# Optimization experiments

Measured on AMD Instinct MI355X. Metric: run time of the kernel, lower is better.

The kernel has to match this reference:

```python
import jax, jax.numpy as jnp
import numpy as np

B, H, W, DIM = 2, 128, 128, 256
NB, EXP, HEADS = 16, 8, 8
BS = DIM // NB          # AFNO block size = 16
DH = DIM // HEADS       # head dim = 32
EPS = 1e-5
LAM = 0.01              # softshrink threshold


def _ln(x, g, b):
    mu = jnp.mean(x, axis=-1, keepdims=True)
    var = jnp.mean((x - mu) ** 2, axis=-1, keepdims=True)
    return (x - mu) * jax.lax.rsqrt(var + EPS) * g + b


def _afno(x, w1, b1, w2, b2):
    # FourCastNet AFNO2D: block-diagonal complex MLP in Fourier space
    bias = x
    Bx, Hx, Wx, C = x.shape
    xf = jnp.fft.rfft2(x, axes=(1, 2), norm='ortho')          # [B,H,W//2+1,C] complex
    xf = xf.reshape(Bx, Hx, Wx // 2 + 1, NB, BS)
    xr, xi = jnp.real(xf), jnp.imag(xf)
    mm = lambda t, w: jnp.einsum('bhwni,nio->bhwno', t, w)
    o1r = jax.nn.relu(mm(xr, w1[0]) - mm(xi, w1[1]) + b1[0])
    o1i = jax.nn.relu(mm(xi, w1[0]) + mm(xr, w1[1]) + b1[1])
    o2r = mm(o1r, w2[0]) - mm(o1i, w2[1]) + b2[0]
    o2i = mm(o1i, w2[0]) + mm(o1r, w2[1]) + b2[1]
    shrink = lambda t: jnp.sign(t) * jnp.maximum(jnp.abs(t) - LAM, 0.0)
    xf = (shrink(o2r) + 1j * shrink(o2i)).reshape(Bx, Hx, Wx // 2 + 1, C)
    out = jnp.fft.irfft2(xf, s=(Hx, Wx), axes=(1, 2), norm='ortho')
    return out + bias


def _galerkin(h, wq, bq, wk, bk, wv, bv, lnk_g, lnk_b, lnv_g, lnv_b, wo, bo):
    # softmax-free linear attention: Q (LN(K)^T LN(V)) / N
    Bx, N, C = h.shape
    split = lambda t, w, b: (t @ w.T + b).reshape(Bx, N, HEADS, DH).transpose(0, 2, 1, 3)
    q = split(h, wq, bq)
    k = split(h, wk, bk)
    v = split(h, wv, bv)
    k = _ln(k, lnk_g[None, :, None, :], lnk_b[None, :, None, :])
    v = _ln(v, lnv_g[None, :, None, :], lnv_b[None, :, None, :])
    kv = jnp.einsum('bhnd,bhne->bhde', k, v) / N     # [B,h,dh,dh]
    out = jnp.einsum('bhnd,bhde->bhne', q, kv)       # [B,h,N,dh]
    out = out.transpose(0, 2, 1, 3).reshape(Bx, N, C)
    return out @ wo.T + bo


def _forward(x, afno_w1, afno_b1, afno_w2, afno_b2,
             wq, bq, wk, bk, wv, bv, lnk_g, lnk_b, lnv_g, lnv_b, wo, bo,
             w_up, b_up, w_down, b_down,
             n1_g, n1_b, n2_g, n2_b, n3_g, n3_b):
    Bx, Hx, Wx, C = x.shape
    # 1) AFNO spectral mixing block
    x = x + _afno(_ln(x, n1_g, n1_b), afno_w1, afno_b1, afno_w2, afno_b2)
    # 2) Galerkin linear attention block
    x = _ln(x, n2_g, n2_b)
    h = x.reshape(Bx, Hx * Wx, C)
    x = x + _galerkin(h, wq, bq, wk, bk, wv, bv,
                      lnk_g, lnk_b, lnv_g, lnv_b, wo, bo).reshape(Bx, Hx, Wx, C)
    # 3) pointwise-conv (1x1) FFN block; conv1x1 over BCHW == per-token linear in BHWC
    x = _ln(x, n3_g, n3_b)
    h = jax.nn.gelu(x @ w_up.T + b_up, approximate=False)
    x = x + h @ w_down.T + b_down
    return x


def setup_inputs() -> dict:
    key = jax.random.key(0)
    ks = jax.random.split(key, 24)
    r = lambda i, shape, s: jax.random.normal(ks[i], shape, dtype=jnp.float32) * s
    z = lambda shape: jnp.zeros(shape, dtype=jnp.float32)
    o = lambda shape: jnp.ones(shape, dtype=jnp.float32)
    return dict(
        x=r(0, (B, H, W, DIM), 1.0),
        afno_w1=r(1, (2, NB, BS, BS * EXP), 0.02),
        afno_b1=r(2, (2, NB, BS * EXP), 0.02),
        afno_w2=r(3, (2, NB, BS * EXP, BS), 0.02),
        afno_b2=r(4, (2, NB, BS), 0.02),
        wq=r(5, (DIM, DIM), 0.02), bq=z((DIM,)),
        wk=r(6, (DIM, DIM), 0.02), bk=z((DIM,)),
        wv=r(7, (DIM, DIM), 0.02), bv=z((DIM,)),
        lnk_g=o((HEADS, DH)), lnk_b=z((HEADS, DH)),
        lnv_g=o((HEADS, DH)), lnv_b=z((HEADS, DH)),
        wo=r(8, (DIM, DIM), 0.02), bo=z((DIM,)),
        w_up=r(9, (DIM * EXP, DIM), 0.02), b_up=z((DIM * EXP,)),
        w_down=r(10, (DIM, DIM * EXP), 0.02), b_down=z((DIM,)),
        n1_g=o((DIM,)), n1_b=z((DIM,)),
        n2_g=o((DIM,)), n2_b=z((DIM,)),
        n3_g=o((DIM,)), n3_b=z((DIM,)),
    )


def reference(x, afno_w1, afno_b1, afno_w2, afno_b2,
              wq, bq, wk, bk, wv, bv, lnk_g, lnk_b, lnv_g, lnv_b, wo, bo,
              w_up, b_up, w_down, b_down,
              n1_g, n1_b, n2_g, n2_b, n3_g, n3_b):
    return _forward(x, afno_w1, afno_b1, afno_w2, afno_b2,
                    wq, bq, wk, bk, wv, bv, lnk_g, lnk_b, lnv_g, lnv_b, wo, bo,
                    w_up, b_up, w_down, b_down,
                    n1_g, n1_b, n2_g, n2_b, n3_g, n3_b)
```

## Files before the change

### kernel.cpp

```cpp
#include <hip/hip_runtime.h>


typedef unsigned short u16;
typedef unsigned int u32;
typedef __attribute__((ext_vector_type(8))) short bf16x8;
typedef __attribute__((ext_vector_type(8))) unsigned short u16x8;
typedef __attribute__((ext_vector_type(4))) float f32x4;
#define DEV __device__ __forceinline__

constexpr int Cch = 256;
constexpr float EPSN = 1e-5f, LAM = 0.01f;
constexpr float TWO_PI = 6.283185307179586f;

DEV float b2f(u16 u) { return __uint_as_float(((u32)u) << 16); }
DEV u16 f2b(float f) {
  u32 x = __float_as_uint(f);
  return (u16)((x + 0x7FFFu + ((x >> 16) & 1u)) >> 16);
}

DEV void put2(u16* tw, int m, int idx, float v) {
  u16 hi = f2b(v);
  tw[m * 16384 + idx] = hi;
  tw[(m + 1) * 16384 + idx] = f2b(v - b2f(hi));
}

__global__ __launch_bounds__(128) void k_twid(u16* __restrict__ tw) {
  int p = blockIdx.x, q = threadIdx.x;
  int idx = p * 128 + q;
  float ang = TWO_PI * (float)((p * q) & 127) * (1.0f / 128.0f);
  float c = cosf(ang), s = sinf(ang);
  put2(tw, 0, idx, c * (1.0f / 128.0f));
  put2(tw, 2, idx, s * (1.0f / 128.0f));
  put2(tw, 4, idx, -s * (1.0f / 128.0f));
  put2(tw, 6, idx, c);
  put2(tw, 8, idx, s);
  put2(tw, 10, idx, -s);
  u16* wmh = tw + 196608;
  u16* wml = tw + 217088;
  for (int k = q; k < 160; k += 128) {
    float v = 0.0f;
    if (k < 65) {
      float sc = (k == 0 || k == 64) ? 1.0f : 2.0f;
      v = sc * cosf(TWO_PI * (float)((p * k) & 127) * (1.0f / 128.0f)) * (1.0f / 128.0f);
    } else if (k < 130) {
      int kk = k - 65;
      float sc = (kk == 0 || kk == 64) ? 1.0f : 2.0f;
      v = -sc * sinf(TWO_PI * (float)((p * kk) & 127) * (1.0f / 128.0f)) * (1.0f / 128.0f);
    }
    u16 hi = f2b(v);
    wmh[p * 160 + k] = hi;
    wml[p * 160 + k] = f2b(v - b2f(hi));
  }
}

__global__ __launch_bounds__(256) void k_wpack(const float* __restrict__ w1,
                                               const float* __restrict__ w2,
                                               u16* __restrict__ W1h, u16* __restrict__ W1l,
                                               u16* __restrict__ W2h, u16* __restrict__ W2l) {
  int idx = blockIdx.x * 256 + threadIdx.x;
  if (idx < 131072) {
    int n = idx >> 13, rem = idx & 8191;
    int out = rem >> 5, k = rem & 31;
    float v;
    if (out < 128)
      v = (k < 16) ? w1[((size_t)n * 16 + k) * 128 + out]
                   : -w1[((size_t)(16 + n) * 16 + (k - 16)) * 128 + out];
    else {
      int o = out - 128;
      v = (k < 16) ? w1[((size_t)(16 + n) * 16 + k) * 128 + o]
                   : w1[((size_t)n * 16 + (k - 16)) * 128 + o];
    }
    u16 hi = f2b(v);
    W1h[idx] = hi; W1l[idx] = f2b(v - b2f(hi));
  } else if (idx < 262144) {
    int id2 = idx - 131072;
    int n = id2 >> 13, rem = id2 & 8191;
    int out2 = rem >> 8, k = rem & 255;
    float v;
    if (out2 < 16)
      v = (k < 128) ? w2[((size_t)n * 128 + k) * 16 + out2]
                    : -w2[((size_t)(16 + n) * 128 + (k - 128)) * 16 + out2];
    else {
      int o = out2 - 16;
      v = (k < 128) ? w2[((size_t)(16 + n) * 128 + k) * 16 + o]
                    : w2[((size_t)n * 128 + (k - 128)) * 16 + o];
    }
    u16 hi = f2b(v);
    W2h[id2] = hi; W2l[id2] = f2b(v - b2f(hi));
  }
}

__global__ __launch_bounds__(256) void k_cvt2(const float* __restrict__ s0,
                                              const float* __restrict__ s1,
                                              u16* __restrict__ d0,
                                              u16* __restrict__ d1, int n) {
  int i = blockIdx.x * 256 + threadIdx.x;
  if (i < n) { d0[i] = f2b(s0[i]); d1[i] = f2b(s1[i]); }
}

template<int INF>
__global__ __launch_bounds__(256) void k_ln(const void* __restrict__ in,
                                            const float* __restrict__ g,
                                            const float* __restrict__ bta,
                                            u16* __restrict__ out) {
  int tid = threadIdx.x, lane = tid & 63;
  size_t token = (size_t)blockIdx.x * 4 + (tid >> 6);
  int c = lane * 4;
  float v[4];
  if (INF) {
    float4 f = *(const float4*)((const float*)in + token * Cch + c);
    v[0] = f.x; v[1] = f.y; v[2] = f.z; v[3] = f.w;
  } else {
    ushort4 u = *(const ushort4*)((const u16*)in + token * Cch + c);
    v[0] = b2f(u.x); v[1] = b2f(u.y); v[2] = b2f(u.z); v[3] = b2f(u.w);
  }
  float s = v[0] + v[1] + v[2] + v[3];
  #pragma unroll
  for (int m = 1; m < 64; m <<= 1) s += __shfl_xor(s, m);
  float mu = s * (1.0f / 256.0f);
  float q = 0.f;
  #pragma unroll
  for (int j = 0; j < 4; j++) { float d = v[j] - mu; q += d * d; }
  #pragma unroll
  for (int m = 1; m < 64; m <<= 1) q += __shfl_xor(q, m);
  float rs = rsqrtf(q * (1.0f / 256.0f) + EPSN);
  ushort4 o;
  o.x = f2b((v[0] - mu) * rs * g[c + 0] + bta[c + 0]);
  o.y = f2b((v[1] - mu) * rs * g[c + 1] + bta[c + 1]);
  o.z = f2b((v[2] - mu) * rs * g[c + 2] + bta[c + 2]);
  o.w = f2b((v[3] - mu) * rs * g[c + 3] + bta[c + 3]);
  *(ushort4*)(out + token * Cch + c) = o;
}

__global__ __launch_bounds__(256) void k_dftw_m(
    const u16* __restrict__ Yg,
    const u16* __restrict__ Chi_, const u16* __restrict__ Clo_,
    const u16* __restrict__ Shi_, const u16* __restrict__ Slo_,
    u16* __restrict__ Or, u16* __restrict__ Oi) {
  __shared__ u16 Bs[128][40];
  int tid = threadIdx.x;
  int bh = blockIdx.x;
  int c0 = blockIdx.y * 128;
  int lane = tid & 63, w = tid >> 6;
  int wm = w >> 1, wn = w & 1;
  int rl = lane & 15, kq = (lane >> 4) * 8, rq = lane >> 4;
  f32x4 accC[4][4] = {};
  f32x4 accS[4][4] = {};
  for (int k0 = 0; k0 < 128; k0 += 32) {
    __syncthreads();
    for (int idx = tid; idx < 1024; idx += 256) {
      int q = idx >> 5, c4 = (idx & 31) * 4;
      ushort4 v = *(const ushort4*)(Yg + ((size_t)bh * 128 + k0 + q) * 256 + c0 + c4);
      Bs[c4 + 0][q] = v.x; Bs[c4 + 1][q] = v.y;
      Bs[c4 + 2][q] = v.z; Bs[c4 + 3][q] = v.w;
    }
    __syncthreads();
    bf16x8 aCh[4], aCl[4], aSh[4], aSl[4], bf[4];
    #pragma unroll
    for (int i = 0; i < 4; i++) {
      int off = (wm * 64 + i * 16 + rl) * 128 + k0 + kq;
      aCh[i] = *(const bf16x8*)(Chi_ + off);
      aCl[i] = *(const bf16x8*)(Clo_ + off);
      aSh[i] = *(const bf16x8*)(Shi_ + off);
      aSl[i] = *(const bf16x8*)(Slo_ + off);
    }
    #pragma unroll
    for (int j = 0; j < 4; j++)
      bf[j] = *(const bf16x8*)&Bs[wn * 64 + j * 16 + rl][kq];
    #pragma unroll
    for (int i = 0; i < 4; i++)
      #pragma unroll
      for (int j = 0; j < 4; j++) {
        accC[i][j] = __builtin_amdgcn_mfma_f32_16x16x32_bf16(aCh[i], bf[j], accC[i][j], 0, 0, 0);
        accC[i][j] = __builtin_amdgcn_mfma_f32_16x16x32_bf16(aCl[i], bf[j], accC[i][j], 0, 0, 0);
        accS[i][j] = __builtin_amdgcn_mfma_f32_16x16x32_bf16(aSh[i], bf[j], accS[i][j], 0, 0, 0);
        accS[i][j] = __builtin_amdgcn_mfma_f32_16x16x32_bf16(aSl[i], bf[j], accS[i][j], 0, 0, 0);
      }
  }
  #pragma unroll
  for (int i = 0; i < 4; i++)
    #pragma unroll
    for (int j = 0; j < 4; j++)
      #pragma unroll
      for (int r = 0; r < 4; r++) {
        int p = wm * 64 + i * 16 + rq * 4 + r;
        if (p < 65) {
          int c = c0 + wn * 64 + j * 16 + rl;
          size_t g = ((size_t)bh * 65 + p) * 256 + c;
          Or[g] = f2b(accC[i][j][r]);
          Oi[g] = f2b(accS[i][j][r]);
        }
      }
}

__global__ __launch_bounds__(256) void k_dfth_m(
    const u16* __restrict__ Br_g, const u16* __restrict__ Bi_g,
    const u16* __restrict__ Chi, const u16* __restrict__ Clo,
    const u16* __restrict__ SRhi, const u16* __restrict__ SRlo,
    const u16* __restrict__ SIhi, const u16* __restrict__ SIlo,
    u16* __restrict__ Or, u16* __restrict__ Oi) {
  __shared__ u16 B1s[128][40], B2s[128][40];
  int tid = threadIdx.x;
  int bk = blockIdx.x;
  int b = bk / 65, kw = bk % 65;
  int c0 = (blockIdx.y & 1) * 128;
  int outI = blockIdx.y >> 1;
  const u16* B1g = outI ? Bi_g : Br_g;
  const u16* B2g = outI ? Br_g : Bi_g;
  const u16* Shi = outI ? SIhi : SRhi;
  const u16* Slo = outI ? SIlo : SRlo;
  u16* outp = outI ? Oi : Or;
  int lane = tid & 63, w = tid >> 6;
  int wm = w >> 1, wn = w & 1;
  int rl = lane & 15, kq = (lane >> 4) * 8, rq = lane >> 4;
  f32x4 acc[4][4] = {};
  for (int k0 = 0; k0 < 128; k0 += 32) {
    __syncthreads();
    for (int idx = tid; idx < 1024; idx += 256) {
      int q = idx >> 5, c4 = (idx & 31) * 4;
      size_t g = (((size_t)b * 128 + k0 + q) * 65 + kw) * 256 + c0 + c4;
      ushort4 v1 = *(const ushort4*)(B1g + g);
      ushort4 v2 = *(const ushort4*)(B2g + g);
      B1s[c4 + 0][q] = v1.x; B1s[c4 + 1][q] = v1.y;
      B1s[c4 + 2][q] = v1.z; B1s[c4 + 3][q] = v1.w;
      B2s[c4 + 0][q] = v2.x; B2s[c4 + 1][q] = v2.y;
      B2s[c4 + 2][q] = v2.z; B2s[c4 + 3][q] = v2.w;
    }
    __syncthreads();
    bf16x8 aCh[4], aCl[4], aSh[4], aSl[4], b1[4], b2[4];
    #pragma unroll
    for (int i = 0; i < 4; i++) {
      int off = (wm * 64 + i * 16 + rl) * 128 + k0 + kq;
      aCh[i] = *(const bf16x8*)(Chi + off);
      aCl[i] = *(const bf16x8*)(Clo + off);
      aSh[i] = *(const bf16x8*)(Shi + off);
      aSl[i] = *(const bf16x8*)(Slo + off);
    }
    #pragma unroll
    for (int j = 0; j < 4; j++) {
      b1[j] = *(const bf16x8*)&B1s[wn * 64 + j * 16 + rl][kq];
      b2[j] = *(const bf16x8*)&B2s[wn * 64 + j * 16 + rl][kq];
    }
    #pragma unroll
    for (int i = 0; i < 4; i++)
      #pragma unroll
      for (int j = 0; j < 4; j++) {
        acc[i][j] = __builtin_amdgcn_mfma_f32_16x16x32_bf16(aCh[i], b1[j], acc[i][j], 0, 0, 0);
        acc[i][j] = __builtin_amdgcn_mfma_f32_16x16x32_bf16(aCl[i], b1[j], acc[i][j], 0, 0, 0);
        acc[i][j] = __builtin_amdgcn_mfma_f32_16x16x32_bf16(aSh[i], b2[j], acc[i][j], 0, 0, 0);
        acc[i][j] = __builtin_amdgcn_mfma_f32_16x16x32_bf16(aSl[i], b2[j], acc[i][j], 0, 0, 0);
      }
  }
  #pragma unroll
  for (int i = 0; i < 4; i++)
    #pragma unroll
    for (int j = 0; j < 4; j++)
      #pragma unroll
      for (int r = 0; r < 4; r++) {
        int p = wm * 64 + i * 16 + rq * 4 + r;
        int c = c0 + wn * 64 + j * 16 + rl;
        outp[(((size_t)b * 128 + p) * 65 + kw) * 256 + c] = f2b(acc[i][j][r]);
      }
}

__global__ __launch_bounds__(256) void k_irfft_m(
    const u16* __restrict__ Ur, const u16* __restrict__ Ui,
    const u16* __restrict__ Whi, const u16* __restrict__ Wlo,
    const float* __restrict__ x_in, const u16* __restrict__ lnout,
    u16* __restrict__ X1) {
  __shared__ u16 Bs[128][40];
  int tid = threadIdx.x;
  int bh = blockIdx.x;
  int c0 = blockIdx.y * 128;
  int lane = tid & 63, w = tid >> 6;
  int wm = w >> 1, wn = w & 1;
  int rl = lane & 15, kq = (lane >> 4) * 8, rq = lane >> 4;
  f32x4 acc[4][4] = {};
  for (int k0 = 0; k0 < 160; k0 += 32) {
    __syncthreads();
    for (int idx = tid; idx < 1024; idx += 256) {
      int q = idx >> 5, c4 = (idx & 31) * 4;
      int grow = k0 + q;
      ushort4 v;
      if (grow < 65)
        v = *(const ushort4*)(Ur + ((size_t)bh * 65 + grow) * 256 + c0 + c4);
      else if (grow < 130)
        v = *(const ushort4*)(Ui + ((size_t)bh * 65 + grow - 65) * 256 + c0 + c4);
      else
        v = make_ushort4(0, 0, 0, 0);
      Bs[c4 + 0][q] = v.x; Bs[c4 + 1][q] = v.y;
      Bs[c4 + 2][q] = v.z; Bs[c4 + 3][q] = v.w;
    }
    __syncthreads();
    bf16x8 ah[4], al[4], bf[4];
    #pragma unroll
    for (int i = 0; i < 4; i++) {
      int off = (wm * 64 + i * 16 + rl) * 160 + k0 + kq;
      ah[i] = *(const bf16x8*)(Whi + off);
      al[i] = *(const bf16x8*)(Wlo + off);
    }
    #pragma unroll
    for (int j = 0; j < 4; j++)
      bf[j] = *(const bf16x8*)&Bs[wn * 64 + j * 16 + rl][kq];
    #pragma unroll
    for (int i = 0; i < 4; i++)
      #pragma unroll
      for (int j = 0; j < 4; j++) {
        acc[i][j] = __builtin_amdgcn_mfma_f32_16x16x32_bf16(ah[i], bf[j], acc[i][j], 0, 0, 0);
        acc[i][j] = __builtin_amdgcn_mfma_f32_16x16x32_bf16(al[i], bf[j], acc[i][j], 0, 0, 0);
      }
  }
  #pragma unroll
  for (int i = 0; i < 4; i++)
    #pragma unroll
    for (int j = 0; j < 4; j++)
      #pragma unroll
      for (int r = 0; r < 4; r++) {
        int p = wm * 64 + i * 16 + rq * 4 + r;
        int c = c0 + wn * 64 + j * 16 + rl;
        size_t g = ((size_t)bh * 128 + p) * 256 + c;
        X1[g] = f2b(x_in[g] + b2f(lnout[g]) + acc[i][j][r]);
      }
}

__global__ __launch_bounds__(256) void k_afno_mfma(
    const u16* __restrict__ Zr, const u16* __restrict__ Zi,
    const u16* __restrict__ W1h, const u16* __restrict__ W1l,
    const u16* __restrict__ W2h, const u16* __restrict__ W2l,
    const float* __restrict__ b1, const float* __restrict__ b2,
    u16* __restrict__ Or, u16* __restrict__ Oi) {
  __shared__ u16 o1buf[4][64][74];
  int tid = threadIdx.x;
  int lane = tid & 63, w = tid >> 6;
  int n = blockIdx.x * 4 + w;
  int p0 = blockIdx.y * 64;
  int rl = lane & 15, rq = lane >> 4, kq = rq * 8;
  bf16x8 bfr[4];
  #pragma unroll
  for (int j = 0; j < 4; j++) {
    int p = p0 + j * 16 + rl;
    const u16* src = (kq < 16) ? (Zr + (size_t)p * 256 + n * 16 + kq)
                               : (Zi + (size_t)p * 256 + n * 16 + kq - 16);
    bfr[j] = *(const bf16x8*)src;
  }
  f32x4 acc2[2][4] = {};
  for (int c = 0; c < 4; c++) {
    f32x4 a1[4][4] = {};
    #pragma unroll
    for (int i = 0; i < 4; i++) {
      int out = c * 64 + i * 16 + rl;
      bf16x8 ah = *(const bf16x8*)(W1h + ((size_t)n * 256 + out) * 32 + kq);
      bf16x8 al = *(const bf16x8*)(W1l + ((size_t)n * 256 + out) * 32 + kq);
      #pragma unroll
      for (int j = 0; j < 4; j++) {
        a1[i][j] = __builtin_amdgcn_mfma_f32_16x16x32_bf16(ah, bfr[j], a1[i][j], 0, 0, 0);
        a1[i][j] = __builtin_amdgcn_mfma_f32_16x16x32_bf16(al, bfr[j], a1[i][j], 0, 0, 0);
      }
    }
    #pragma unroll
    for (int i = 0; i < 4; i++) {
      float bv[4];
      #pragma unroll
      for (int r = 0; r < 4; r++) {
        int out = c * 64 + i * 16 + rq * 4 + r;
        bv[r] = (out < 128) ? b1[n * 128 + out] : b1[2048 + n * 128 + out - 128];
      }
      #pragma unroll
      for (int j = 0; j < 4; j++) {
        ushort4 pk;
        u16* pp = &pk.x;
        #pragma unroll
        for (int r = 0; r < 4; r++)
          pp[r] = f2b(fmaxf(a1[i][j][r] + bv[r], 0.0f));
        *(ushort4*)&o1buf[w][j * 16 + rl][i * 16 + rq * 4] = pk;
      }
    }
    #pragma unroll
    for (int ks = 0; ks < 2; ks++) {
      int kg = c * 64 + ks * 32 + kq;
      #pragma unroll
      for (int i2 = 0; i2 < 2; i2++) {
        int out2 = i2 * 16 + rl;
        bf16x8 ah = *(const bf16x8*)(W2h + ((size_t)n * 32 + out2) * 256 + kg);
        bf16x8 al = *(const bf16x8*)(W2l + ((size_t)n * 32 + out2) * 256 + kg);
        #pragma unroll
        for (int j = 0; j < 4; j++) {
          bf16x8 bb = *(const bf16x8*)&o1buf[w][j * 16 + rl][ks * 32 + kq];
          acc2[i2][j] = __builtin_amdgcn_mfma_f32_16x16x32_bf16(ah, bb, acc2[i2][j], 0, 0, 0);
          acc2[i2][j] = __builtin_amdgcn_mfma_f32_16x16x32_bf16(al, bb, acc2[i2][j], 0, 0, 0);
        }
      }
    }
  }
  #pragma unroll
  for (int i2 = 0; i2 < 2; i2++)
    #pragma unroll
    for (int r = 0; r < 4; r++) {
      int out2 = i2 * 16 + rq * 4 + r;
      float bv = (out2 < 16) ? b2[n * 16 + out2] : b2[256 + n * 16 + out2 - 16];
      int ch = (out2 < 16) ? out2 : out2 - 16;
      #pragma unroll
      for (int j = 0; j < 4; j++) {
        float v = acc2[i2][j][r] + bv;
        v = copysignf(fmaxf(fabsf(v) - LAM, 0.0f), v);
        size_t g = (size_t)(p0 + j * 16 + rl) * 256 + n * 16 + ch;
        if (out2 < 16) Or[g] = f2b(v);
        else Oi[g] = f2b(v);
      }
    }
}

template<int ACT, int RT, int OUTF>
__global__ __launch_bounds__(256) void k_mgemm(const u16* __restrict__ Ap,
                                               const u16* __restrict__ Bp,
                                               const float* __restrict__ bias,
                                               const u16* __restrict__ resid,
                                               void* __restrict__ Cp,
                                               int M, int N, int K) {
  __shared__ u16 As[128][40];
  __shared__ u16 Bs[128][40];
  int tid = threadIdx.x;
  int lane = tid & 63, w = tid >> 6;
  int wm = w >> 1, wn = w & 1;
  int m0 = blockIdx.x * 128, n0 = blockIdx.y * 128;
  int srow = tid >> 1, sseg = tid & 1;
  const u16* ag = Ap + (size_t)(m0 + srow) * K + sseg * 16;
  const u16* bg = Bp + (size_t)(n0 + srow) * K + sseg * 16;
  int rl = lane & 15, kq = (lane >> 4) * 8;
  f32x4 acc[4][4] = {};
  for (int k0 = 0; k0 < K; k0 += 32) {
    __syncthreads();
    *(u16x8*)&As[srow][sseg * 16]     = *(const u16x8*)(ag + k0);
    *(u16x8*)&As[srow][sseg * 16 + 8] = *(const u16x8*)(ag + k0 + 8);
    *(u16x8*)&Bs[srow][sseg * 16]     = *(const u16x8*)(bg + k0);
    *(u16x8*)&Bs[srow][sseg * 16 + 8] = *(const u16x8*)(bg + k0 + 8);
    __syncthreads();
    bf16x8 af[4], bf[4];
    #pragma unroll
    for (int i = 0; i < 4; i++) {
      af[i] = *(const bf16x8*)&As[wm * 64 + i * 16 + rl][kq];
      bf[i] = *(const bf16x8*)&Bs[wn * 64 + i * 16 + rl][kq];
    }
    #pragma unroll
    for (int i = 0; i < 4; i++)
      #pragma unroll
      for (int j = 0; j < 4; j++)
        acc[i][j] = __builtin_amdgcn_mfma_f32_16x16x32_bf16(af[i], bf[j], acc[i][j], 0, 0, 0);
  }
  int rq = lane >> 4;
  #pragma unroll
  for (int i = 0; i < 4; i++) {
    #pragma unroll
    for (int j = 0; j < 4; j++) {
      #pragma unroll
      for (int r = 0; r < 4; r++) {
        int m = m0 + wm * 64 + i * 16 + rq * 4 + r;
        int n = n0 + wn * 64 + j * 16 + rl;
        float v = acc[i][j][r] + bias[n];
        if (ACT) v = 0.5f * v * (1.0f + erff(v * 0.70710678118654752f));
        if (RT) v += b2f(resid[(size_t)m * N + n]);
        if (OUTF) ((float*)Cp)[(size_t)m * N + n] = v;
        else ((u16*)Cp)[(size_t)m * N + n] = f2b(v);
      }
    }
  }
}

__global__ __launch_bounds__(256) void k_lnhead(u16* __restrict__ X,
                                                const float* __restrict__ g,
                                                const float* __restrict__ bta) {
  int tid = threadIdx.x, lane = tid & 63;
  size_t token = (size_t)blockIdx.x * 4 + (tid >> 6);
  int c = lane * 4;
  ushort4 u = *(const ushort4*)(X + token * Cch + c);
  float v[4] = {b2f(u.x), b2f(u.y), b2f(u.z), b2f(u.w)};
  float s = v[0] + v[1] + v[2] + v[3];
  s += __shfl_xor(s, 1); s += __shfl_xor(s, 2); s += __shfl_xor(s, 4);
  float mu = s * (1.0f / 32.0f);
  float q = 0.f;
  #pragma unroll
  for (int j = 0; j < 4; j++) { float d = v[j] - mu; q += d * d; }
  q += __shfl_xor(q, 1); q += __shfl_xor(q, 2); q += __shfl_xor(q, 4);
  float rs = rsqrtf(q * (1.0f / 32.0f) + EPSN);
  ushort4 o;
  o.x = f2b((v[0] - mu) * rs * g[c + 0] + bta[c + 0]);
  o.y = f2b((v[1] - mu) * rs * g[c + 1] + bta[c + 1]);
  o.z = f2b((v[2] - mu) * rs * g[c + 2] + bta[c + 2]);
  o.w = f2b((v[3] - mu) * rs * g[c + 3] + bta[c + 3]);
  *(ushort4*)(X + token * Cch + c) = o;
}

__global__ __launch_bounds__(256) void k_kv_partial(const u16* __restrict__ Kb,
                                                    const u16* __restrict__ Vb,
                                                    float* __restrict__ part) {
  __shared__ float kl[64][33], vl[64][33];
  int tid = threadIdx.x;
  int bh = blockIdx.x;
  int b = bh >> 3, h = bh & 7;
  int n0 = blockIdx.y * 1024;
  int d = tid >> 3, eg = tid & 7;
  float acc[4] = {0.f, 0.f, 0.f, 0.f};
  for (int sub = 0; sub < 16; sub++) {
    __syncthreads();
    for (int idx = tid; idx < 64 * 32; idx += 256) {
      int nn = idx >> 5, c = idx & 31;
      size_t o = ((size_t)(b * 16384 + n0 + sub * 64 + nn)) * Cch + h * 32 + c;
      kl[nn][c] = b2f(Kb[o]); vl[nn][c] = b2f(Vb[o]);
    }
    __syncthreads();
    #pragma unroll 4
    for (int nn = 0; nn < 64; nn++) {
      float kd = kl[nn][d];
      #pragma unroll
      for (int j = 0; j < 4; j++) acc[j] += kd * vl[nn][eg * 4 + j];
    }
  }
  size_t base = ((size_t)bh * 16 + blockIdx.y) * 1024 + d * 32 + eg * 4;
  #pragma unroll
  for (int j = 0; j < 4; j++) part[base + j] = acc[j];
}

__global__ __launch_bounds__(1024) void k_kv_reduce(const float* __restrict__ part,
                                                    u16* __restrict__ kvTh,
                                                    u16* __restrict__ kvTl) {
  int bh = blockIdx.x, o = threadIdx.x;
  float s = 0.f;
  #pragma unroll
  for (int p = 0; p < 16; p++) s += part[((size_t)bh * 16 + p) * 1024 + o];
  s *= (1.0f / 16384.0f);
  int d = o >> 5, e = o & 31;
  u16 hi = f2b(s);
  kvTh[(size_t)bh * 1024 + e * 32 + d] = hi;
  kvTl[(size_t)bh * 1024 + e * 32 + d] = f2b(s - b2f(hi));
}

__global__ __launch_bounds__(256) void k_attn_m(const u16* __restrict__ Q,
                                                const u16* __restrict__ kvTh,
                                                const u16* __restrict__ kvTl,
                                                u16* __restrict__ ATT) {
  int tid = threadIdx.x;
  int lane = tid & 63, w = tid >> 6;
  int h = blockIdx.y;
  int t0 = blockIdx.x * 64 + w * 16;
  int b = t0 >> 14;
  int rl = lane & 15, rq = lane >> 4, kq = rq * 8;
  bf16x8 a = *(const bf16x8*)(Q + (size_t)(t0 + rl) * 256 + h * 32 + kq);
  const u16* kh = kvTh + (size_t)(b * 8 + h) * 1024;
  const u16* kl = kvTl + (size_t)(b * 8 + h) * 1024;
  f32x4 acc[2] = {};
  #pragma unroll
  for (int j = 0; j < 2; j++) {
    bf16x8 bh_ = *(const bf16x8*)(kh + (j * 16 + rl) * 32 + kq);
    bf16x8 bl_ = *(const bf16x8*)(kl + (j * 16 + rl) * 32 + kq);
    acc[j] = __builtin_amdgcn_mfma_f32_16x16x32_bf16(a, bh_, acc[j], 0, 0, 0);
    acc[j] = __builtin_amdgcn_mfma_f32_16x16x32_bf16(a, bl_, acc[j], 0, 0, 0);
  }
  #pragma unroll
  for (int j = 0; j < 2; j++)
    #pragma unroll
    for (int r = 0; r < 4; r++)
      ATT[(size_t)(t0 + rq * 4 + r) * 256 + h * 32 + j * 16 + rl] = f2b(acc[j][r]);
}

extern "C" void kernel_launch(void* const* d_in, const int* in_sizes, int n_in,
                              void* d_out, int out_size, void* d_ws, size_t ws_size,
                              hipStream_t stream) {
  (void)in_sizes; (void)n_in; (void)out_size; (void)ws_size;
  const float* x    = (const float*)d_in[0];
  const float* w1   = (const float*)d_in[1];
  const float* b1   = (const float*)d_in[2];
  const float* w2   = (const float*)d_in[3];
  const float* b2   = (const float*)d_in[4];
  const float* wq   = (const float*)d_in[5];
  const float* bq   = (const float*)d_in[6];
  const float* wk   = (const float*)d_in[7];
  const float* bk   = (const float*)d_in[8];
  const float* wv   = (const float*)d_in[9];
  const float* bv   = (const float*)d_in[10];
  const float* lnkg = (const float*)d_in[11];
  const float* lnkb = (const float*)d_in[12];
  const float* lnvg = (const float*)d_in[13];
  const float* lnvb = (const float*)d_in[14];
  const float* wo   = (const float*)d_in[15];
  const float* bo   = (const float*)d_in[16];
  const float* wup  = (const float*)d_in[17];
  const float* bup  = (const float*)d_in[18];
  const float* wdn  = (const float*)d_in[19];
  const float* bdn  = (const float*)d_in[20];
  const float* n1g  = (const float*)d_in[21];
  const float* n1b  = (const float*)d_in[22];
  const float* n2g  = (const float*)d_in[23];
  const float* n2b  = (const float*)d_in[24];
  const float* n3g  = (const float*)d_in[25];
  const float* n3b  = (const float*)d_in[26];

  char* ws = (char*)d_ws;
  u16* A    = (u16*)(ws + 0);
  u16* S1r  = (u16*)(ws + 16777216);
  u16* S1i  = (u16*)(ws + 25296896);
  u16* S2r  = (u16*)(ws + 33816576);
  u16* S2i  = (u16*)(ws + 42336256);
  u16* X1   = (u16*)(ws + 16777216);
  u16* Vb   = (u16*)(ws + 16777216);
  u16* Qb   = (u16*)(ws + 16777216);
  u16* X2   = (u16*)(ws + 16777216);
  u16* Kb   = (u16*)(ws + 33816576);
  u16* ATT  = (u16*)(ws + 33816576);
  u16* UP   = (u16*)(ws + 33816576);
  u16* wq_b = (u16*)(ws + 33554432);
  u16* wk_b = (u16*)(ws + 33685504);
  u16* wv_b = (u16*)(ws + 50593792);
  u16* wo_b = (u16*)(ws + 50724864);
  u16* wup_b = (u16*)(ws + 16777216);
  u16* wdn_b = (u16*)(ws + 17825792);
  u16* TW   = (u16*)(ws + 50855936);
  float* KVp = (float*)(ws + 50855936);
  u16* kvTh = (u16*)(ws + 51904512);
  u16* kvTl = (u16*)(ws + 51937280);
  float* outp = (float*)d_out;
  u16* W1h = (u16*)d_out;
  u16* W1l = W1h + 131072;
  u16* W2h = W1h + 262144;
  u16* W2l = W1h + 393216;

  u16 *Cf_h = TW + 0 * 16384, *Cf_l = TW + 1 * 16384;
  u16 *Sf_h = TW + 2 * 16384, *Sf_l = TW + 3 * 16384;
  u16 *Snf_h = TW + 4 * 16384, *Snf_l = TW + 5 * 16384;
  u16 *Cu_h = TW + 6 * 16384, *Cu_l = TW + 7 * 16384;
  u16 *Su_h = TW + 8 * 16384, *Su_l = TW + 9 * 16384;
  u16 *Snu_h = TW + 10 * 16384, *Snu_l = TW + 11 * 16384;
  u16 *Wm_h = TW + 196608, *Wm_l = TW + 217088;

  k_twid<<<128, 128, 0, stream>>>(TW);
  k_wpack<<<1024, 256, 0, stream>>>(w1, w2, W1h, W1l, W2h, W2l);

  k_ln<1><<<8192, 256, 0, stream>>>((const void*)x, n1g, n1b, A);
  k_dftw_m<<<dim3(256, 2), 256, 0, stream>>>(A, Cu_h, Cu_l, Snu_h, Snu_l, S1r, S1i);
  k_dfth_m<<<dim3(130, 4), 256, 0, stream>>>(S1r, S1i, Cf_h, Cf_l, Sf_h, Sf_l, Snf_h, Snf_l, S2r, S2i);
  k_afno_mfma<<<dim3(4, 260), 256, 0, stream>>>(S2r, S2i, W1h, W1l, W2h, W2l, b1, b2, S1r, S1i);
  k_dfth_m<<<dim3(130, 4), 256, 0, stream>>>(S1r, S1i, Cu_h, Cu_l, Snu_h, Snu_l, Su_h, Su_l, S2r, S2i);
  k_irfft_m<<<dim3(256, 2), 256, 0, stream>>>(S2r, S2i, Wm_h, Wm_l, x, A, X1);

  k_cvt2<<<256, 256, 0, stream>>>(wq, wk, wq_b, wk_b, 65536);
  k_cvt2<<<256, 256, 0, stream>>>(wv, wo, wv_b, wo_b, 65536);

  k_ln<0><<<8192, 256, 0, stream>>>((const void*)X1, n2g, n2b, A);
  k_mgemm<0, 0, 0><<<dim3(256, 2), 256, 0, stream>>>(A, wk_b, bk, nullptr, (void*)Kb, 32768, 256, 256);
  k_mgemm<0, 0, 0><<<dim3(256, 2), 256, 0, stream>>>(A, wv_b, bv, nullptr, (void*)Vb, 32768, 256, 256);
  k_lnhead<<<8192, 256, 0, stream>>>(Kb, lnkg, lnkb);
  k_lnhead<<<8192, 256, 0, stream>>>(Vb, lnvg, lnvb);
  k_kv_partial<<<dim3(16, 16), 256, 0, stream>>>(Kb, Vb, KVp);
  k_kv_reduce<<<16, 1024, 0, stream>>>(KVp, kvTh, kvTl);
  k_mgemm<0, 0, 0><<<dim3(256, 2), 256, 0, stream>>>(A, wq_b, bq, nullptr, (void*)Qb, 32768, 256, 256);
  k_attn_m<<<dim3(512, 8), 256, 0, stream>>>(Qb, kvTh, kvTl, ATT);
  k_mgemm<0, 1, 0><<<dim3(256, 2), 256, 0, stream>>>(ATT, wo_b, bo, A, (void*)X2, 32768, 256, 256);

  k_ln<0><<<8192, 256, 0, stream>>>((const void*)X2, n3g, n3b, A);
  k_cvt2<<<2048, 256, 0, stream>>>(wup, wdn, wup_b, wdn_b, 524288);
  for (int c = 0; c < 8; c++) {
    const u16* Ac = A + (size_t)c * 4096 * 256;
    k_mgemm<1, 0, 0><<<dim3(32, 16), 256, 0, stream>>>(Ac, wup_b, bup, nullptr, (void*)UP, 4096, 2048, 256);
    k_mgemm<0, 1, 1><<<dim3(32, 2), 256, 0, stream>>>(UP, wdn_b, bdn, Ac, (void*)(outp + (size_t)c * 4096 * 256), 4096, 256, 2048);
  }
}
```

Baseline: 902.7 us.

## Fuse QKV GEMMs and head LNs, swizzle AFNO LDS, retile down-projection GEMM

Replaces three separate Q/K/V projection launches with one grid that picks the weight, bias and output per blockIdx.y. It merges the two per-head LayerNorm launches into one 2-D grid and moves the Q buffer into the output allocation so all three projections can be written together. The down-projection GEMM moves from 64 blocks with 128x128 tiles to 256 blocks with 64x64 tiles, to fill more compute units on the K=2048 reduction. The AFNO hidden-activation LDS buffer gets an XOR swizzle to reduce bank conflicts. The smaller tiles cost more redundant global loads per output element.

```diff
diff --git a/kernel.cpp b/kernel.cpp
--- a/kernel.cpp
+++ b/kernel.cpp
@@ -367,12 +367,13 @@
       }
       #pragma unroll
       for (int j = 0; j < 4; j++) {
+        int pos = j * 16 + rl;
         ushort4 pk;
         u16* pp = &pk.x;
         #pragma unroll
         for (int r = 0; r < 4; r++)
           pp[r] = f2b(fmaxf(a1[i][j][r] + bv[r], 0.0f));
-        *(ushort4*)&o1buf[w][j * 16 + rl][i * 16 + rq * 4] = pk;
+        *(ushort4*)&o1buf[w][pos][(i * 16 + rq * 4) ^ ((pos & 7) << 3)] = pk;
       }
     }
     #pragma unroll
@@ -385,7 +386,8 @@
         bf16x8 al = *(const bf16x8*)(W2l + ((size_t)n * 32 + out2) * 256 + kg);
         #pragma unroll
         for (int j = 0; j < 4; j++) {
-          bf16x8 bb = *(const bf16x8*)&o1buf[w][j * 16 + rl][ks * 32 + kq];
+          int pos = j * 16 + rl;
+          bf16x8 bb = *(const bf16x8*)&o1buf[w][pos][(ks * 32 + kq) ^ ((pos & 7) << 3)];
           acc2[i2][j] = __builtin_amdgcn_mfma_f32_16x16x32_bf16(ah, bb, acc2[i2][j], 0, 0, 0);
           acc2[i2][j] = __builtin_amdgcn_mfma_f32_16x16x32_bf16(al, bb, acc2[i2][j], 0, 0, 0);
         }
@@ -466,10 +468,116 @@
   }
 }
 
-__global__ __launch_bounds__(256) void k_lnhead(u16* __restrict__ X,
-                                                const float* __restrict__ g,
-                                                const float* __restrict__ bta) {
+__global__ __launch_bounds__(256) void k_mgemm_qkv(
+    const u16* __restrict__ Ap,
+    const u16* __restrict__ Wk, const u16* __restrict__ Wv, const u16* __restrict__ Wq,
+    const float* __restrict__ bk, const float* __restrict__ bv, const float* __restrict__ bq,
+    u16* __restrict__ Ko, u16* __restrict__ Vo, u16* __restrict__ Qo) {
+  __shared__ u16 As[128][40];
+  __shared__ u16 Bs[128][40];
+  int sel = blockIdx.y >> 1;
+  const u16* Bp = (sel == 0) ? Wk : (sel == 1) ? Wv : Wq;
+  const float* bias = (sel == 0) ? bk : (sel == 1) ? bv : bq;
+  u16* Cp = (sel == 0) ? Ko : (sel == 1) ? Vo : Qo;
+  int tid = threadIdx.x;
+  int lane = tid & 63, w = tid >> 6;
+  int wm = w >> 1, wn = w & 1;
+  int m0 = blockIdx.x * 128, n0 = (blockIdx.y & 1) * 128;
+  int srow = tid >> 1, sseg = tid & 1;
+  const u16* ag = Ap + (size_t)(m0 + srow) * 256 + sseg * 16;
+  const u16* bg = Bp + (size_t)(n0 + srow) * 256 + sseg * 16;
+  int rl = lane & 15, kq = (lane >> 4) * 8;
+  f32x4 acc[4][4] = {};
+  for (int k0 = 0; k0 < 256; k0 += 32) {
+    __syncthreads();
+    *(u16x8*)&As[srow][sseg * 16]     = *(const u16x8*)(ag + k0);
+    *(u16x8*)&As[srow][sseg * 16 + 8] = *(const u16x8*)(ag + k0 + 8);
+    *(u16x8*)&Bs[srow][sseg * 16]     = *(const u16x8*)(bg + k0);
+    *(u16x8*)&Bs[srow][sseg * 16 + 8] = *(const u16x8*)(bg + k0 + 8);
+    __syncthreads();
+    bf16x8 af[4], bf[4];
+    #pragma unroll
+    for (int i = 0; i < 4; i++) {
+      af[i] = *(const bf16x8*)&As[wm * 64 + i * 16 + rl][kq];
+      bf[i] = *(const bf16x8*)&Bs[wn * 64 + i * 16 + rl][kq];
+    }
+    #pragma unroll
+    for (int i = 0; i < 4; i++)
+      #pragma unroll
+      for (int j = 0; j < 4; j++)
+        acc[i][j] = __builtin_amdgcn_mfma_f32_16x16x32_bf16(af[i], bf[j], acc[i][j], 0, 0, 0);
+  }
+  int rq = lane >> 4;
+  #pragma unroll
+  for (int i = 0; i < 4; i++)
+    #pragma unroll
+    for (int j = 0; j < 4; j++)
+      #pragma unroll
+      for (int r = 0; r < 4; r++) {
+        int m = m0 + wm * 64 + i * 16 + rq * 4 + r;
+        int n = n0 + wn * 64 + j * 16 + rl;
+        Cp[(size_t)m * 256 + n] = f2b(acc[i][j][r] + bias[n]);
+      }
+}
+
+__global__ __launch_bounds__(256) void k_mgemm_d(const u16* __restrict__ Ap,
+                                                 const u16* __restrict__ Bp,
+                                                 const float* __restrict__ bias,
+                                                 const u16* __restrict__ resid,
+                                                 float* __restrict__ Cp,
+                                                 int M, int N, int K) {
+  __shared__ u16 As[64][40];
+  __shared__ u16 Bs[64][40];
+  int tid = threadIdx.x;
+  int lane = tid & 63, w = tid >> 6;
+  int wm = w >> 1, wn = w & 1;
+  int m0 = blockIdx.x * 64, n0 = blockIdx.y * 64;
+  int srow = tid >> 2, sseg = tid & 3;
+  const u16* ag = Ap + (size_t)(m0 + srow) * K + sseg * 8;
+  const u16* bg = Bp + (size_t)(n0 + srow) * K + sseg * 8;
+  int rl = lane & 15, kq = (lane >> 4) * 8;
+  f32x4 acc[2][2] = {};
+  for (int k0 = 0; k0 < K; k0 += 32) {
+    __syncthreads();
+    *(u16x8*)&As[srow][sseg * 8] = *(const u16x8*)(ag + k0);
+    *(u16x8*)&Bs[srow][sseg * 8] = *(const u16x8*)(bg + k0);
+    __syncthreads();
+    bf16x8 af[2], bf[2];
+    #pragma unroll
+    for (int i = 0; i < 2; i++) {
+      af[i] = *(const bf16x8*)&As[wm * 32 + i * 16 + rl][kq];
+      bf[i] = *(const bf16x8*)&Bs[wn * 32 + i * 16 + rl][kq];
+    }
+    #pragma unroll
+    for (int i = 0; i < 2; i++)
+      #pragma unroll
+      for (int j = 0; j < 2; j++)
+        acc[i][j] = __builtin_amdgcn_mfma_f32_16x16x32_bf16(af[i], bf[j], acc[i][j], 0, 0, 0);
+  }
+  int rq = lane >> 4;
+  #pragma unroll
+  for (int i = 0; i < 2; i++)
+    #pragma unroll
+    for (int j = 0; j < 2; j++)
+      #pragma unroll
+      for (int r = 0; r < 4; r++) {
+        int m = m0 + wm * 32 + i * 16 + rq * 4 + r;
+        int n = n0 + wn * 32 + j * 16 + rl;
+        float v = acc[i][j][r] + bias[n] + b2f(resid[(size_t)m * N + n]);
+        Cp[(size_t)m * N + n] = v;
+      }
+}
+
+__global__ __launch_bounds__(256) void k_lnhead2(u16* __restrict__ K,
+                                                 u16* __restrict__ V,
+                                                 const float* __restrict__ kg,
+                                                 const float* __restrict__ kb,
+                                                 const float* __restrict__ vg,
+                                                 const float* __restrict__ vb) {
   int tid = threadIdx.x, lane = tid & 63;
+  u16* X = blockIdx.y ? V : K;
+  const float* g = blockIdx.y ? vg : kg;
+  const float* bta = blockIdx.y ? vb : kb;
   size_t token = (size_t)blockIdx.x * 4 + (tid >> 6);
   int c = lane * 4;
   ushort4 u = *(const ushort4*)(X + token * Cch + c);
@@ -602,7 +710,6 @@
   u16* S2i  = (u16*)(ws + 42336256);
   u16* X1   = (u16*)(ws + 16777216);
   u16* Vb   = (u16*)(ws + 16777216);
-  u16* Qb   = (u16*)(ws + 16777216);
   u16* X2   = (u16*)(ws + 16777216);
   u16* Kb   = (u16*)(ws + 33816576);
   u16* ATT  = (u16*)(ws + 33816576);
@@ -618,6 +725,7 @@
   u16* kvTh = (u16*)(ws + 51904512);
   u16* kvTl = (u16*)(ws + 51937280);
   float* outp = (float*)d_out;
+  u16* Qb  = (u16*)d_out;
   u16* W1h = (u16*)d_out;
   u16* W1l = W1h + 131072;
   u16* W2h = W1h + 262144;
@@ -645,13 +753,10 @@
   k_cvt2<<<256, 256, 0, stream>>>(wv, wo, wv_b, wo_b, 65536);
 
   k_ln<0><<<8192, 256, 0, stream>>>((const void*)X1, n2g, n2b, A);
-  k_mgemm<0, 0, 0><<<dim3(256, 2), 256, 0, stream>>>(A, wk_b, bk, nullptr, (void*)Kb, 32768, 256, 256);
-  k_mgemm<0, 0, 0><<<dim3(256, 2), 256, 0, stream>>>(A, wv_b, bv, nullptr, (void*)Vb, 32768, 256, 256);
-  k_lnhead<<<8192, 256, 0, stream>>>(Kb, lnkg, lnkb);
-  k_lnhead<<<8192, 256, 0, stream>>>(Vb, lnvg, lnvb);
+  k_mgemm_qkv<<<dim3(256, 6), 256, 0, stream>>>(A, wk_b, wv_b, wq_b, bk, bv, bq, Kb, Vb, Qb);
+  k_lnhead2<<<dim3(8192, 2), 256, 0, stream>>>(Kb, Vb, lnkg, lnkb, lnvg, lnvb);
   k_kv_partial<<<dim3(16, 16), 256, 0, stream>>>(Kb, Vb, KVp);
   k_kv_reduce<<<16, 1024, 0, stream>>>(KVp, kvTh, kvTl);
-  k_mgemm<0, 0, 0><<<dim3(256, 2), 256, 0, stream>>>(A, wq_b, bq, nullptr, (void*)Qb, 32768, 256, 256);
   k_attn_m<<<dim3(512, 8), 256, 0, stream>>>(Qb, kvTh, kvTl, ATT);
   k_mgemm<0, 1, 0><<<dim3(256, 2), 256, 0, stream>>>(ATT, wo_b, bo, A, (void*)X2, 32768, 256, 256);
 
@@ -660,6 +765,6 @@
   for (int c = 0; c < 8; c++) {
     const u16* Ac = A + (size_t)c * 4096 * 256;
     k_mgemm<1, 0, 0><<<dim3(32, 16), 256, 0, stream>>>(Ac, wup_b, bup, nullptr, (void*)UP, 4096, 2048, 256);
-    k_mgemm<0, 1, 1><<<dim3(32, 2), 256, 0, stream>>>(UP, wdn_b, bdn, Ac, (void*)(outp + (size_t)c * 4096 * 256), 4096, 256, 2048);
-  }
-}
+    k_mgemm_d<<<dim3(64, 4), 256, 0, stream>>>(UP, wdn_b, bdn, Ac, outp + (size_t)c * 4096 * 256, 4096, 256, 2048);
+  }
+}
```

Measured after the change: 743.0 us. 17.7% less time.
